# Performance work log

Hardware: AMD Instinct MI355X
Metric: run time of the kernel (lower is better)

Reference implementation:

```python
import jax, jax.numpy as jnp
import numpy as np

NUM_EMB = 512
EMB_DIM = 64
BETA = 0.25


def _conv(x, w, b, stride, pad):
    # x: NCHW, w: OIHW
    y = jax.lax.conv_general_dilated(
        x, w, window_strides=(stride, stride),
        padding=[(pad, pad), (pad, pad)],
        dimension_numbers=('NCHW', 'OIHW', 'NCHW'))
    return y + b[None, :, None, None]


def _deconv(x, w, b, stride, pad, k):
    # torch ConvTranspose2d weight is [in, out, kh, kw]; flip spatially,
    # swap to OIHW, and run a fractionally-strided (lhs-dilated) conv.
    wt = jnp.flip(w, axis=(2, 3)).transpose(1, 0, 2, 3)
    p = k - 1 - pad
    y = jax.lax.conv_general_dilated(
        x, wt, window_strides=(1, 1),
        padding=[(p, p), (p, p)],
        lhs_dilation=(stride, stride),
        dimension_numbers=('NCHW', 'OIHW', 'NCHW'))
    return y + b[None, :, None, None]


def setup_inputs() -> dict:
    key = jax.random.key(0)
    ks = jax.random.split(key, 16)
    s = 0.05
    inp = {
        'x': jax.random.normal(ks[0], (32, 3, 256, 256), jnp.float32),
        # encoder
        'w1': jax.random.normal(ks[1], (64, 3, 4, 4), jnp.float32) * s,
        'b1': jnp.zeros((64,), jnp.float32),
        'w2': jax.random.normal(ks[2], (128, 64, 4, 4), jnp.float32) * s,
        'b2': jnp.zeros((128,), jnp.float32),
        'w3': jax.random.normal(ks[3], (EMB_DIM, 128, 3, 3), jnp.float32) * s,
        'b3': jnp.zeros((EMB_DIM,), jnp.float32),
        # codebook, uniform(-1/N, 1/N) as in torch init
        'emb': jax.random.uniform(ks[4], (NUM_EMB, EMB_DIM), jnp.float32,
                                  -1.0 / NUM_EMB, 1.0 / NUM_EMB),
        # decoder (ConvTranspose2d weights: [in, out, kh, kw])
        'dw1': jax.random.normal(ks[5], (EMB_DIM, 128, 4, 4), jnp.float32) * s,
        'db1': jnp.zeros((128,), jnp.float32),
        'dw2': jax.random.normal(ks[6], (128, 64, 4, 4), jnp.float32) * s,
        'db2': jnp.zeros((64,), jnp.float32),
        'dw3': jax.random.normal(ks[7], (64, 3, 3, 3), jnp.float32) * s,
        'db3': jnp.zeros((3,), jnp.float32),
    }
    return inp


def _forward(x, w1, b1, w2, b2, w3, b3, emb, dw1, db1, dw2, db2, dw3, db3):
    # encoder
    h = jax.nn.relu(_conv(x, w1, b1, 2, 1))
    h = jax.nn.relu(_conv(h, w2, b2, 2, 1))
    z = jax.nn.relu(_conv(h, w3, b3, 1, 1))      # [B, D, H/4, W/4]
    z = z.transpose(0, 2, 3, 1)                   # NHWC
    # vector quantize
    flat = z.reshape(-1, EMB_DIM)                 # [N, D]
    d = (jnp.sum(flat * flat, axis=1, keepdims=True)
         - 2.0 * flat @ emb.T
         + jnp.sum(emb * emb, axis=1))            # [N, K]
    idx = jnp.argmin(d, axis=1)
    q = emb[idx].reshape(z.shape)
    sg = jax.lax.stop_gradient
    loss = jnp.mean((sg(q) - z) ** 2) + BETA * jnp.mean((q - sg(z)) ** 2)
    q = z + sg(q - z)                             # straight-through
    q = q.transpose(0, 3, 1, 2)                   # NCHW
    # decoder
    h = jax.nn.relu(_deconv(q, dw1, db1, 2, 1, 4))
    h = jax.nn.relu(_deconv(h, dw2, db2, 2, 1, 4))
    x_recon = jax.nn.sigmoid(_deconv(h, dw3, db3, 1, 1, 3))
    return x_recon, loss


def reference(x, w1, b1, w2, b2, w3, b3, emb, dw1, db1, dw2, db2, dw3, db3):
    return _forward(x, w1, b1, w2, b2, w3, b3, emb,
                    dw1, db1, dw2, db2, dw3, db3)
```

## Files before the change

### kernel.cpp

```cpp
#include <hip/hip_runtime.h>
#include <math.h>


typedef __attribute__((ext_vector_type(8))) short bf16x8;
typedef __attribute__((ext_vector_type(4))) float fx4;
typedef unsigned short ushort_t;
#define MFMA16(a, b, c) __builtin_amdgcn_mfma_f32_16x16x32_bf16(a, b, c, 0, 0, 0)

__device__ inline ushort_t f2bf(float f) {
    unsigned u = __float_as_uint(f);
    u += 0x7FFFu + ((u >> 16) & 1u);
    return (ushort_t)(u >> 16);
}
__device__ inline float bf2f(ushort_t h) {
    return __uint_as_float(((unsigned)h) << 16);
}

__device__ __forceinline__ void stage16(const ushort_t* g, ushort_t* l) {
#if __has_builtin(__builtin_amdgcn_global_load_lds)
    __builtin_amdgcn_global_load_lds(
        (const __attribute__((address_space(1))) unsigned int*)g,
        (__attribute__((address_space(3))) unsigned int*)l, 16, 0, 0);
#else
    int lane = threadIdx.x & 63;
    *(int4*)(l + lane * 8) = *(const int4*)g;
#endif
}

__device__ __forceinline__ int swz(int s) { return s ^ ((s >> 3) & 7); }
__device__ __forceinline__ bf16x8 sld(const ushort_t* sm, int gslot) {
    return *(const bf16x8*)(sm + (size_t)swz(gslot) * 8);
}

__device__ __forceinline__ void halo_do(
    ushort_t* __restrict__ buf, int B, int H, int W, int C8, int idx)
{
    int perim = 2 * W + 2 * (H - 2);
    int c8 = idx % C8;
    int t = idx / C8;
    int p = t % perim;
    int b = t / perim;
    int r, col;
    if (p < W) { r = 0; col = p; }
    else if (p < 2 * W) { r = H - 1; col = p - W; }
    else { int pp = p - 2 * W; r = 1 + (pp >> 1); col = (pp & 1) ? (W - 1) : 0; }
    size_t off = ((((size_t)b * H + r) * W + col) * C8 + c8) * 8;
    *(int4*)(buf + off) = (int4){0, 0, 0, 0};
}

__global__ __launch_bounds__(256) void halo3_k(
    ushort_t* __restrict__ xp, ushort_t* __restrict__ h2p, ushort_t* __restrict__ qpad)
{
    int i = blockIdx.x * 256 + threadIdx.x;
    if (i < 132096) halo_do(xp, 32, 130, 130, 8, i);
    else if (i < 265216) halo_do(h2p, 32, 66, 66, 16, i - 132096);
    else if (i < 331776) halo_do(qpad, 32, 66, 66, 8, i - 265216);
}
__global__ __launch_bounds__(256) void halo2_k(
    ushort_t* __restrict__ d1c, ushort_t* __restrict__ d2c)
{
    int i = blockIdx.x * 256 + threadIdx.x;
    if (i < 132096) halo_do(d1c, 16, 130, 130, 16, i);
    else if (i < 263680) halo_do(d2c, 16, 258, 258, 8, i - 132096);
}

__global__ __launch_bounds__(256) void cast_x4(
    const float* __restrict__ x, ushort_t* __restrict__ x4)
{
    if (blockIdx.x < 8192) {
        int i = blockIdx.x * 256 + threadIdx.x;
        int w = i & 255, h = (i >> 8) & 255, b = i >> 16;
        size_t base = ((size_t)b * 3 * 256 + h) * 256 + w;
        float v0 = x[base];
        float v1 = x[base + 65536];
        float v2 = x[base + 131072];
        uint2 o;
        o.x = (unsigned)f2bf(v0) | ((unsigned)f2bf(v1) << 16);
        o.y = (unsigned)f2bf(v2);
        *(uint2*)(x4 + ((size_t)(b * 258 + h + 1) * 258 + (w + 1)) * 4) = o;
    } else {
        int idx = (blockIdx.x - 8192) * 256 + threadIdx.x;
        if (idx >= 32 * 1032) return;
        int b = idx / 1032;
        int s = idx % 1032;
        int side = s / 258, c = s % 258;
        int r, col;
        if (side == 0) { r = 0; col = c; }
        else if (side == 1) { r = 257; col = c; }
        else if (side == 2) { r = c; col = 0; }
        else { r = c; col = 257; }
        *(uint2*)(x4 + ((size_t)(b * 258 + r) * 258 + col) * 4) = (uint2){0, 0};
    }
}

__global__ __launch_bounds__(256) void repack_all(
    const float* __restrict__ w1, const float* __restrict__ w2,
    const float* __restrict__ w3, const float* __restrict__ dw1,
    const float* __restrict__ dw2, const float* __restrict__ dw3,
    const float* __restrict__ emb,
    ushort_t* __restrict__ o1, ushort_t* __restrict__ o2,
    ushort_t* __restrict__ o3, ushort_t* __restrict__ od1,
    ushort_t* __restrict__ od2, ushort_t* __restrict__ od3,
    ushort_t* __restrict__ embb, float* __restrict__ se2,
    float* __restrict__ lac)
{
    int gi = blockIdx.x * 256 + threadIdx.x;
    if (gi < 4096) {
        int i = gi;
        int j = i & 7, lane = (i >> 3) & 63, tc = i >> 9;
        int c = tc & 1, t = tc >> 1;
        int co = t * 16 + (lane & 15);
        int k = c * 32 + (lane >> 4) * 8 + j;
        int kh = k >> 4, kw = (k >> 2) & 3, ci = k & 3;
        o1[i] = (ci < 3) ? f2bf(w1[((co * 3 + ci) * 4 + kh) * 4 + kw]) : (ushort_t)0;
    } else if (gi < 135168) {
        int i = gi - 4096;
        int j = i & 7, lane = (i >> 3) & 63, tc = i >> 9;
        int c = tc & 31, t = tc >> 5;
        int co = t * 16 + (lane & 15);
        int k = c * 32 + (lane >> 4) * 8 + j;
        int tap = k >> 6, ci = k & 63, kh = tap >> 2, kw = tap & 3;
        o2[i] = f2bf(w2[((co * 64 + ci) * 4 + kh) * 4 + kw]);
    } else if (gi < 208896) {
        int i = gi - 135168;
        int j = i & 7, lane = (i >> 3) & 63, tc = i >> 9;
        int c = tc % 36, t = tc / 36;
        int co = t * 16 + (lane & 15);
        int k = c * 32 + (lane >> 4) * 8 + j;
        int tap = k >> 7, ci = k & 127, kh = tap / 3, kw = tap % 3;
        o3[i] = f2bf(w3[((co * 128 + ci) * 3 + kh) * 3 + kw]);
    } else if (gi < 339968) {
        int i = gi - 208896;
        int j = i & 7, lane = (i >> 3) & 63, tc = i >> 9;
        int c = tc & 31, t = tc >> 5;
        int co = t * 16 + (lane & 15);
        int k = c * 32 + (lane >> 4) * 8 + j;
        int tap = k >> 6, ci = k & 63, kh = tap >> 2, kw = tap & 3;
        od1[i] = f2bf(dw1[((ci * 128 + co) * 4 + kh) * 4 + kw]);
    } else if (gi < 471040) {
        int i = gi - 339968;
        int j = i & 7, lane = (i >> 3) & 63, tc = i >> 9;
        int c = tc & 63, t = tc >> 6;
        int co = t * 16 + (lane & 15);
        int k = c * 32 + (lane >> 4) * 8 + j;
        int tap = k >> 7, ci = k & 127, kh = tap >> 2, kw = tap & 3;
        od2[i] = f2bf(dw2[((ci * 64 + co) * 4 + kh) * 4 + kw]);
    } else if (gi < 480256) {
        int i = gi - 471040;
        int j = i & 7, lane = (i >> 3) & 63, c = i >> 9;
        int co = lane & 15;
        int k = c * 32 + (lane >> 4) * 8 + j;
        int tap = k >> 6, ci = k & 63, kh = tap / 3, kw = tap % 3;
        od3[i] = (co < 3) ? f2bf(dw3[((ci * 3 + co) * 3 + kh) * 3 + kw]) : (ushort_t)0;
    } else if (gi < 513024) {
        int i = gi - 480256;
        int j = i & 7, lane = (i >> 3) & 63, c = (i >> 9) & 1, nt = i >> 10;
        int n = nt * 16 + (lane & 15);
        int k = c * 32 + (lane >> 4) * 8 + j;
        embb[i] = f2bf(emb[n * 64 + k]);
    } else if (gi < 513536) {
        int n = gi - 513024;
        const float* e = emb + n * 64;
        float s = 0.f;
        for (int d = 0; d < 64; ++d) s = fmaf(e[d], e[d], s);
        se2[n] = s;
    } else if (gi == 513536) {
        lac[0] = 0.f;
    }
}

__global__ __launch_bounds__(256) void conv1_mfma(
    const ushort_t* __restrict__ x4, const ushort_t* __restrict__ wr,
    const float* __restrict__ bias, ushort_t* __restrict__ xp)
{
    __shared__ ushort_t sm[4608];
    int tid = threadIdx.x;
    int wv = tid >> 6, lane = tid & 63;
    int n16 = lane & 15, quad = lane >> 4;
    int blk = blockIdx.x;
    int oh = blk & 127, b = blk >> 7;
    const ushort_t* gsrc = x4 + (size_t)(b * 258 + 2 * oh) * 1032;
    int sl = lane ^ ((lane >> 3) & 7);
    bf16x8 bfr[4][2];
    #pragma unroll
    for (int nt = 0; nt < 4; ++nt)
        #pragma unroll
        for (int c = 0; c < 2; ++c)
            bfr[nt][c] = *(const bf16x8*)(wr + ((size_t)(nt * 2 + c) * 64 + lane) * 8);
    for (int u = wv; u < 9; u += 4)
        stage16(gsrc + u * 512 + sl * 8, sm + u * 512);
    __syncthreads();

    fx4 acc[2][4];
    #pragma unroll
    for (int i = 0; i < 2; ++i)
        #pragma unroll
        for (int j = 0; j < 4; ++j) acc[i][j] = (fx4){0.f, 0.f, 0.f, 0.f};
    #pragma unroll
    for (int c = 0; c < 2; ++c) {
        int kh = 2 * c + (quad >> 1);
        int kwh = quad & 1;
        bf16x8 af[2];
        #pragma unroll
        for (int mt = 0; mt < 2; ++mt) {
            int ow = (wv * 2 + mt) * 16 + n16;
            af[mt] = sld(sm, kh * 129 + ow + kwh);
        }
        #pragma unroll
        for (int mt = 0; mt < 2; ++mt)
            #pragma unroll
            for (int nt = 0; nt < 4; ++nt)
                acc[mt][nt] = MFMA16(af[mt], bfr[nt][c], acc[mt][nt]);
    }
    #pragma unroll
    for (int nt = 0; nt < 4; ++nt) {
        int co = nt * 16 + n16;
        float bs = bias[co];
        #pragma unroll
        for (int mt = 0; mt < 2; ++mt) {
            #pragma unroll
            for (int r = 0; r < 4; ++r) {
                int ow = (wv * 2 + mt) * 16 + quad * 4 + r;
                xp[((size_t)(b * 130 + oh + 1) * 130 + (ow + 1)) * 64 + co] =
                    f2bf(fmaxf(acc[mt][nt][r] + bs, 0.f));
            }
        }
    }
}

__global__ __launch_bounds__(256, 2) void conv2_mfma(
    const ushort_t* __restrict__ xp, const ushort_t* __restrict__ wr,
    const float* __restrict__ bias, ushort_t* __restrict__ h2p)
{
    __shared__ ushort_t sm[33280];
    int tid = threadIdx.x;
    int wv = tid >> 6, lane = tid & 63;
    int n16 = lane & 15, quad = lane >> 4;
    int blk = blockIdx.x;
    int oh = blk & 63, b = blk >> 6;
    const ushort_t* gsrc = xp + (size_t)(b * 130 + 2 * oh) * 130 * 64;
    int sl = lane ^ ((lane >> 3) & 7);
    const ushort_t* w0 = wr + ((size_t)(wv * 2 + 0) * 32 * 64 + lane) * 8;
    const ushort_t* w1 = wr + ((size_t)(wv * 2 + 1) * 32 * 64 + lane) * 8;

    bf16x8 Bq[2][16];
    #pragma unroll
    for (int s = 0; s < 8; ++s) {
        Bq[0][2 * s]     = *(const bf16x8*)(w0 + (size_t)s * 512);
        Bq[0][2 * s + 1] = *(const bf16x8*)(w1 + (size_t)s * 512);
    }
    for (int u = wv; u < 65; u += 4)
        stage16(gsrc + (size_t)u * 512 + sl * 8, sm + u * 512);
    __syncthreads();

    fx4 acc[4][2];
    #pragma unroll
    for (int i = 0; i < 4; ++i)
        #pragma unroll
        for (int j = 0; j < 2; ++j) acc[i][j] = (fx4){0.f, 0.f, 0.f, 0.f};
    #pragma unroll
    for (int qb = 0; qb < 4; ++qb) {
        int cur = qb & 1;
        if (qb < 3) {
            #pragma unroll
            for (int s = 0; s < 8; ++s) {
                int st = (qb + 1) * 8 + s;
                Bq[cur ^ 1][2 * s]     = *(const bf16x8*)(w0 + (size_t)st * 512);
                Bq[cur ^ 1][2 * s + 1] = *(const bf16x8*)(w1 + (size_t)st * 512);
            }
        }
        #pragma unroll
        for (int s = 0; s < 8; ++s) {
            int step = qb * 8 + s, tap = step >> 1, ks = step & 1;
            int kh = tap >> 2, kw = tap & 3;
            bf16x8 af[4];
            #pragma unroll
            for (int mt = 0; mt < 4; ++mt) {
                int px = kw + 2 * (mt * 16 + n16);
                af[mt] = sld(sm, (kh * 130 + px) * 8 + ks * 4 + quad);
            }
            #pragma unroll
            for (int mt = 0; mt < 4; ++mt) {
                acc[mt][0] = MFMA16(af[mt], Bq[cur][2 * s], acc[mt][0]);
                acc[mt][1] = MFMA16(af[mt], Bq[cur][2 * s + 1], acc[mt][1]);
            }
        }
    }
    #pragma unroll
    for (int nt = 0; nt < 2; ++nt) {
        int co = (wv * 2 + nt) * 16 + n16;
        float bs = bias[co];
        #pragma unroll
        for (int mt = 0; mt < 4; ++mt) {
            #pragma unroll
            for (int r = 0; r < 4; ++r) {
                int ow = mt * 16 + quad * 4 + r;
                h2p[((size_t)(b * 66 + oh + 1) * 66 + (ow + 1)) * 128 + co] =
                    f2bf(fmaxf(acc[mt][nt][r] + bs, 0.f));
            }
        }
    }
}

__global__ __launch_bounds__(256, 2) void conv3_mfma(
    const ushort_t* __restrict__ hp, const ushort_t* __restrict__ wr,
    const float* __restrict__ bias, ushort_t* __restrict__ z)
{
    __shared__ ushort_t sm[25600];
    int tid = threadIdx.x;
    int wv = tid >> 6, lane = tid & 63;
    int n16 = lane & 15, quad = lane >> 4;
    int blk = blockIdx.x;
    int oh = blk & 63, b = blk >> 6;
    const ushort_t* gsrc = hp + (size_t)(b * 66 + oh) * 66 * 128;
    int sl = lane ^ ((lane >> 3) & 7);
    const ushort_t* wb = wr + ((size_t)wv * 36 * 64 + lane) * 8;
    bf16x8 Bb[36];
    #pragma unroll
    for (int s = 0; s < 36; ++s)
        Bb[s] = *(const bf16x8*)(wb + (size_t)s * 512);
    for (int u = wv; u < 50; u += 4)
        stage16(gsrc + (size_t)u * 512 + sl * 8, sm + u * 512);
    __syncthreads();

    fx4 acc[4];
    #pragma unroll
    for (int i = 0; i < 4; ++i) acc[i] = (fx4){0.f, 0.f, 0.f, 0.f};
    #pragma unroll
    for (int tap = 0; tap < 9; ++tap) {
        int kh = tap / 3, kw = tap % 3;
        #pragma unroll
        for (int ks = 0; ks < 4; ++ks) {
            bf16x8 af[4];
            #pragma unroll
            for (int mt = 0; mt < 4; ++mt) {
                int px = kw + mt * 16 + n16;
                af[mt] = sld(sm, (kh * 66 + px) * 16 + ks * 4 + quad);
            }
            #pragma unroll
            for (int mt = 0; mt < 4; ++mt)
                acc[mt] = MFMA16(af[mt], Bb[tap * 4 + ks], acc[mt]);
        }
    }
    int co = wv * 16 + n16;
    float bs = bias[co];
    #pragma unroll
    for (int mt = 0; mt < 4; ++mt) {
        #pragma unroll
        for (int r = 0; r < 4; ++r) {
            int ow = mt * 16 + quad * 4 + r;
            z[((size_t)(b * 64 + oh) * 64 + ow) * 64 + co] =
                f2bf(fmaxf(acc[mt][r] + bs, 0.f));
        }
    }
}

__global__ __launch_bounds__(256) void vq_mfma(
    const ushort_t* __restrict__ z, const ushort_t* __restrict__ embb,
    const float* __restrict__ emb, const float* __restrict__ se2g,
    ushort_t* __restrict__ qpad, float* __restrict__ loss_acc)
{
    __shared__ ushort_t smz[16384];
    __shared__ float sse2[512];
    __shared__ float red[256];
    int tid = threadIdx.x;
    int wv = tid >> 6, lane = tid & 63;
    int n16 = lane & 15, quad = lane >> 4;
    int blk = blockIdx.x;
    const ushort_t* gsrc = z + (size_t)blk * 16384;
    int sl = lane ^ ((lane >> 3) & 7);
    for (int u = wv; u < 32; u += 4)
        stage16(gsrc + (size_t)u * 512 + sl * 8, smz + u * 512);
    for (int i = tid; i < 512; i += 256) sse2[i] = se2g[i];
    __syncthreads();

    bf16x8 a[4][2];
    #pragma unroll
    for (int mt = 0; mt < 4; ++mt)
        #pragma unroll
        for (int ks = 0; ks < 2; ++ks)
            a[mt][ks] = sld(smz, (wv * 64 + mt * 16 + n16) * 8 + ks * 4 + quad);

    float best[4][4];
    int bid[4][4];
    #pragma unroll
    for (int mt = 0; mt < 4; ++mt)
        #pragma unroll
        for (int r = 0; r < 4; ++r) { best[mt][r] = 1e30f; bid[mt][r] = 0; }

    for (int nt = 0; nt < 32; ++nt) {
        bf16x8 b0 = *(const bf16x8*)(embb + ((size_t)(nt * 2 + 0) * 64 + lane) * 8);
        bf16x8 b1 = *(const bf16x8*)(embb + ((size_t)(nt * 2 + 1) * 64 + lane) * 8);
        float s2 = sse2[nt * 16 + n16];
        int myn = nt * 16 + n16;
        #pragma unroll
        for (int mt = 0; mt < 4; ++mt) {
            fx4 acc = (fx4){0.f, 0.f, 0.f, 0.f};
            acc = MFMA16(a[mt][0], b0, acc);
            acc = MFMA16(a[mt][1], b1, acc);
            #pragma unroll
            for (int r = 0; r < 4; ++r) {
                float sc = fmaf(-2.f, acc[r], s2);
                if (sc < best[mt][r]) { best[mt][r] = sc; bid[mt][r] = myn; }
            }
        }
    }

    float lsum = 0.f;
    #pragma unroll
    for (int mt = 0; mt < 4; ++mt) {
        #pragma unroll
        for (int r = 0; r < 4; ++r) {
            float bs = best[mt][r];
            int bi = bid[mt][r];
            #pragma unroll
            for (int st = 1; st < 16; st <<= 1) {
                float os = __shfl_xor(bs, st, 64);
                int oi = __shfl_xor(bi, st, 64);
                if (os < bs || (os == bs && oi < bi)) { bs = os; bi = oi; }
            }
            int ml = wv * 64 + mt * 16 + quad * 4 + r;
            int pos = blk * 256 + ml;
            int b = pos >> 12, h = (pos >> 6) & 63, w = pos & 63;
            float4 ev = *(const float4*)(emb + (size_t)bi * 64 + n16 * 4);
            int slot = ml * 8 + (n16 >> 1);
            const ushort_t* zp = smz + (size_t)swz(slot) * 8 + (n16 & 1) * 4;
            float d0 = ev.x - bf2f(zp[0]);
            float d1 = ev.y - bf2f(zp[1]);
            float d2 = ev.z - bf2f(zp[2]);
            float d3 = ev.w - bf2f(zp[3]);
            lsum = fmaf(d0, d0, lsum);
            lsum = fmaf(d1, d1, lsum);
            lsum = fmaf(d2, d2, lsum);
            lsum = fmaf(d3, d3, lsum);
            uint2 o;
            o.x = (unsigned)f2bf(ev.x) | ((unsigned)f2bf(ev.y) << 16);
            o.y = (unsigned)f2bf(ev.z) | ((unsigned)f2bf(ev.w) << 16);
            *(uint2*)(qpad + ((size_t)(b * 66 + h + 1) * 66 + (w + 1)) * 64 + n16 * 4) = o;
        }
    }
    red[tid] = lsum;
    __syncthreads();
    for (int s = 128; s > 0; s >>= 1) {
        if (tid < s) red[tid] += red[tid + s];
        __syncthreads();
    }
    if (tid == 0) atomicAdd(loss_acc, red[0]);
}

__global__ void loss_fin_k(const float* __restrict__ acc, float* __restrict__ out)
{
    out[0] = 1.25f * acc[0] / 8388608.0f;
}

__global__ __launch_bounds__(256, 2) void deconv1_mfma(
    const ushort_t* __restrict__ q, const ushort_t* __restrict__ wr,
    const float* __restrict__ bias, ushort_t* __restrict__ d1)
{
    __shared__ ushort_t sm[8704];
    int tid = threadIdx.x;
    int wv = tid >> 6, lane = tid & 63;
    int n16 = lane & 15, quad = lane >> 4;
    int blk = blockIdx.x;
    int oh = blk & 127, b = blk >> 7;
    int h0 = (oh + 1) & 1;
    int ihp0 = ((oh + 1 - h0) >> 1) + 1;
    const ushort_t* gsrc = q + (size_t)(b * 66 + ihp0 - 1) * 66 * 64;
    int sl = lane ^ ((lane >> 3) & 7);
    int pw = wv & 1, ng = wv >> 1;
    int q0 = 1 - pw;
    bf16x8 Bb[4][8];
    #pragma unroll
    for (int nt = 0; nt < 4; ++nt) {
        const ushort_t* wb = wr + ((size_t)(ng * 4 + nt) * 32 * 64 + lane) * 8;
        #pragma unroll
        for (int t2 = 0; t2 < 2; ++t2)
            #pragma unroll
            for (int t3 = 0; t3 < 2; ++t3)
                #pragma unroll
                for (int ks = 0; ks < 2; ++ks) {
                    int tap = (h0 + 2 * t2) * 4 + (q0 + 2 * t3);
                    Bb[nt][t2 * 4 + t3 * 2 + ks] =
                        *(const bf16x8*)(wb + (size_t)(tap * 2 + ks) * 512);
                }
    }
    for (int u = wv; u < 17; u += 4)
        stage16(gsrc + (size_t)u * 512 + sl * 8, sm + u * 512);
    __syncthreads();

    fx4 acc[4][4];
    #pragma unroll
    for (int i = 0; i < 4; ++i)
        #pragma unroll
        for (int j = 0; j < 4; ++j) acc[i][j] = (fx4){0.f, 0.f, 0.f, 0.f};
    #pragma unroll
    for (int t2 = 0; t2 < 2; ++t2) {
        int lrow = 1 - t2;
        #pragma unroll
        for (int t3 = 0; t3 < 2; ++t3) {
            int cadd = pw + (t3 == 0 ? 1 : 0);
            #pragma unroll
            for (int ks = 0; ks < 2; ++ks) {
                bf16x8 af[4];
                #pragma unroll
                for (int mt = 0; mt < 4; ++mt) {
                    int px = cadd + mt * 16 + n16;
                    af[mt] = sld(sm, (lrow * 66 + px) * 8 + ks * 4 + quad);
                }
                #pragma unroll
                for (int mt = 0; mt < 4; ++mt)
                    #pragma unroll
                    for (int nt = 0; nt < 4; ++nt)
                        acc[mt][nt] = MFMA16(af[mt], Bb[nt][t2 * 4 + t3 * 2 + ks], acc[mt][nt]);
            }
        }
    }
    #pragma unroll
    for (int nt = 0; nt < 4; ++nt) {
        int co = (ng * 4 + nt) * 16 + n16;
        float bs = bias[co];
        #pragma unroll
        for (int mt = 0; mt < 4; ++mt) {
            #pragma unroll
            for (int r = 0; r < 4; ++r) {
                int ow = 2 * (mt * 16 + quad * 4 + r) + pw;
                d1[((size_t)(b * 130 + oh + 1) * 130 + (ow + 1)) * 128 + co] =
                    f2bf(fmaxf(acc[mt][nt][r] + bs, 0.f));
            }
        }
    }
}

__global__ __launch_bounds__(256, 2) void deconv2_mfma(
    const ushort_t* __restrict__ d1, const ushort_t* __restrict__ wr,
    const float* __restrict__ bias, ushort_t* __restrict__ d2)
{
    __shared__ ushort_t sm[33280];
    int tid = threadIdx.x;
    int wv = tid >> 6, lane = tid & 63;
    int n16 = lane & 15, quad = lane >> 4;
    int blk = blockIdx.x;
    int oh = blk & 255, b = blk >> 8;
    int h0 = (oh + 1) & 1;
    int ihp0 = ((oh + 1 - h0) >> 1) + 1;
    const ushort_t* gsrc = d1 + (size_t)(b * 130 + ihp0 - 1) * 130 * 128;
    int sl = lane ^ ((lane >> 3) & 7);
    int pw = wv & 1, ng = wv >> 1;
    int q0 = 1 - pw;
    bf16x8 Bb[2][16];
    #pragma unroll
    for (int nt = 0; nt < 2; ++nt) {
        const ushort_t* wb = wr + ((size_t)(ng * 2 + nt) * 64 * 64 + lane) * 8;
        #pragma unroll
        for (int t2 = 0; t2 < 2; ++t2)
            #pragma unroll
            for (int t3 = 0; t3 < 2; ++t3) {
                int tap = (h0 + 2 * t2) * 4 + (q0 + 2 * t3);
                #pragma unroll
                for (int ks = 0; ks < 4; ++ks)
                    Bb[nt][t2 * 8 + t3 * 4 + ks] =
                        *(const bf16x8*)(wb + (size_t)(tap * 4 + ks) * 512);
            }
    }
    for (int u = wv; u < 65; u += 4)
        stage16(gsrc + (size_t)u * 512 + sl * 8, sm + u * 512);
    __syncthreads();

    fx4 acc[8][2];
    #pragma unroll
    for (int i = 0; i < 8; ++i)
        #pragma unroll
        for (int j = 0; j < 2; ++j) acc[i][j] = (fx4){0.f, 0.f, 0.f, 0.f};
    #pragma unroll
    for (int t2 = 0; t2 < 2; ++t2) {
        int lrow = 1 - t2;
        #pragma unroll
        for (int t3 = 0; t3 < 2; ++t3) {
            int cadd = pw + (t3 == 0 ? 1 : 0);
            #pragma unroll
            for (int ks = 0; ks < 4; ++ks) {
                #pragma unroll
                for (int mt = 0; mt < 8; ++mt) {
                    int px = cadd + mt * 16 + n16;
                    bf16x8 af = sld(sm, (lrow * 130 + px) * 16 + ks * 4 + quad);
                    acc[mt][0] = MFMA16(af, Bb[0][t2 * 8 + t3 * 4 + ks], acc[mt][0]);
                    acc[mt][1] = MFMA16(af, Bb[1][t2 * 8 + t3 * 4 + ks], acc[mt][1]);
                }
            }
        }
    }
    #pragma unroll
    for (int nt = 0; nt < 2; ++nt) {
        int co = (ng * 2 + nt) * 16 + n16;
        float bs = bias[co];
        #pragma unroll
        for (int mt = 0; mt < 8; ++mt) {
            #pragma unroll
            for (int r = 0; r < 4; ++r) {
                int ow = 2 * (mt * 16 + quad * 4 + r) + pw;
                d2[((size_t)(b * 258 + oh + 1) * 258 + (ow + 1)) * 64 + co] =
                    f2bf(fmaxf(acc[mt][nt][r] + bs, 0.f));
            }
        }
    }
}

__global__ __launch_bounds__(256) void deconv3_mfma(
    const ushort_t* __restrict__ d2, const ushort_t* __restrict__ wr,
    const float* __restrict__ bias, float* __restrict__ out)
{
    __shared__ ushort_t sm[26112];
    int tid = threadIdx.x;
    int wv = tid >> 6, lane = tid & 63;
    int n16 = lane & 15, quad = lane >> 4;
    int blk = blockIdx.x;
    int half = blk & 1;
    int oh = (blk >> 1) & 255;
    int b = blk >> 9;
    int sl = lane ^ ((lane >> 3) & 7);
    bf16x8 Bb[18];
    #pragma unroll
    for (int s = 0; s < 18; ++s)
        Bb[s] = *(const bf16x8*)(wr + ((size_t)s * 64 + lane) * 8);
    for (int u = wv; u < 51; u += 4) {
        int c = u / 17, uu = u - c * 17;
        const ushort_t* gsrc = d2 + ((size_t)(b * 258 + oh + c) * 258 + half * 128) * 64;
        stage16(gsrc + (size_t)uu * 512 + sl * 8, sm + c * 8704 + uu * 512);
    }
    __syncthreads();

    fx4 acc[2];
    #pragma unroll
    for (int i = 0; i < 2; ++i) acc[i] = (fx4){0.f, 0.f, 0.f, 0.f};
    #pragma unroll
    for (int tap = 0; tap < 9; ++tap) {
        int kh = tap / 3, kw = tap % 3;
        int c = 2 - kh;
        #pragma unroll
        for (int ks = 0; ks < 2; ++ks) {
            bf16x8 af[2];
            #pragma unroll
            for (int mt = 0; mt < 2; ++mt) {
                int px = (2 - kw) + (wv * 2 + mt) * 16 + n16;
                af[mt] = sld(sm, c * 1088 + px * 8 + ks * 4 + quad);
            }
            #pragma unroll
            for (int mt = 0; mt < 2; ++mt)
                acc[mt] = MFMA16(af[mt], Bb[tap * 2 + ks], acc[mt]);
        }
    }
    int co = n16;
    if (co < 3) {
        float bs = bias[co];
        #pragma unroll
        for (int mt = 0; mt < 2; ++mt) {
            int ow0 = half * 128 + (wv * 2 + mt) * 16 + quad * 4;
            float4 v;
            v.x = 1.f / (1.f + __expf(-(acc[mt][0] + bs)));
            v.y = 1.f / (1.f + __expf(-(acc[mt][1] + bs)));
            v.z = 1.f / (1.f + __expf(-(acc[mt][2] + bs)));
            v.w = 1.f / (1.f + __expf(-(acc[mt][3] + bs)));
            *(float4*)(out + (((size_t)b * 3 + co) * 256 + oh) * 256 + ow0) = v;
        }
    }
}

extern "C" void kernel_launch(void* const* d_in, const int* in_sizes, int n_in,
                              void* d_out, int out_size, void* d_ws, size_t ws_size,
                              hipStream_t stream)
{
    const float* x   = (const float*)d_in[0];
    const float* w1  = (const float*)d_in[1];
    const float* b1  = (const float*)d_in[2];
    const float* w2  = (const float*)d_in[3];
    const float* b2  = (const float*)d_in[4];
    const float* w3  = (const float*)d_in[5];
    const float* b3  = (const float*)d_in[6];
    const float* emb = (const float*)d_in[7];
    const float* dw1 = (const float*)d_in[8];
    const float* db1 = (const float*)d_in[9];
    const float* dw2 = (const float*)d_in[10];
    const float* db2 = (const float*)d_in[11];
    const float* dw3 = (const float*)d_in[12];
    const float* db3 = (const float*)d_in[13];
    float* xout = (float*)d_out;

    ushort_t* shared = (ushort_t*)d_ws;
    ushort_t* xp   = shared;
    ushort_t* h2p  = shared + 34611200;
    ushort_t* d1c  = shared;
    ushort_t* d2c  = shared + 34611200;
    ushort_t* x4   = shared + 94252544;
    ushort_t* zb   = shared + 102772736;
    ushort_t* qpad = zb + 8388608;
    ushort_t* wr1  = qpad + 8921088;
    ushort_t* wr2  = wr1  + 4096;
    ushort_t* wr3  = wr2  + 131072;
    ushort_t* wd1  = wr3  + 73728;
    ushort_t* wd2  = wd1  + 131072;
    ushort_t* wd3  = wd2  + 131072;
    ushort_t* embb = wd3  + 9216;
    float*    se2  = (float*)(embb + 32768);
    float*    lac  = se2 + 512;

    repack_all<<<2007, 256, 0, stream>>>(w1, w2, w3, dw1, dw2, dw3, emb,
                                         wr1, wr2, wr3, wd1, wd2, wd3,
                                         embb, se2, lac);
    cast_x4 <<<8321, 256, 0, stream>>>(x, x4);
    halo3_k <<<1296, 256, 0, stream>>>(xp, h2p, qpad);

    conv1_mfma<<<4096, 256, 0, stream>>>(x4, wr1, b1, xp);
    conv2_mfma<<<2048, 256, 0, stream>>>(xp, wr2, b2, h2p);
    conv3_mfma<<<2048, 256, 0, stream>>>(h2p, wr3, b3, zb);
    vq_mfma   <<<512,  256, 0, stream>>>(zb, embb, emb, se2, qpad, lac);
    loss_fin_k<<<1, 1, 0, stream>>>(lac, xout + 6291456);

    halo2_k<<<1030, 256, 0, stream>>>(d1c, d2c);

    for (int c0 = 0; c0 < 32; c0 += 16) {
        deconv1_mfma<<<2048, 256, 0, stream>>>(qpad + (size_t)c0 * 278784, wd1, db1, d1c);
        deconv2_mfma<<<4096, 256, 0, stream>>>(d1c, wd2, db2, d2c);
        deconv3_mfma<<<8192, 256, 0, stream>>>(d2c, wd3, db3, xout + (size_t)c0 * 196608);
    }
}
```

Before: 592.2 us.

## Switch deconv2 to 32x32x16 MFMA with double-buffered per-tap weight loads

Rewrites deconv2 to use 32x32x16 bf16 MFMA tiles. Each wave now covers half the output columns and all 64 output channels, instead of all columns and 32 channels. The dw2 weight prepack layout is changed to match. Weights are loaded per tap into a double-buffered register set, overlapped with compute, rather than all held at once. The accumulator is initialized with the bias. This aims to raise MFMA efficiency and cut register pressure at the cost of more global weight loads per block.

```diff
diff --git a/kernel.cpp b/kernel.cpp
--- a/kernel.cpp
+++ b/kernel.cpp
@@ -4,8 +4,10 @@
 
 typedef __attribute__((ext_vector_type(8))) short bf16x8;
 typedef __attribute__((ext_vector_type(4))) float fx4;
+typedef __attribute__((ext_vector_type(16))) float fx16;
 typedef unsigned short ushort_t;
 #define MFMA16(a, b, c) __builtin_amdgcn_mfma_f32_16x16x32_bf16(a, b, c, 0, 0, 0)
+#define MFMA32(a, b, c) __builtin_amdgcn_mfma_f32_32x32x16_bf16(a, b, c, 0, 0, 0)
 
 __device__ inline ushort_t f2bf(float f) {
     unsigned u = __float_as_uint(f);
@@ -139,11 +141,11 @@
         od1[i] = f2bf(dw1[((ci * 128 + co) * 4 + kh) * 4 + kw]);
     } else if (gi < 471040) {
         int i = gi - 339968;
-        int j = i & 7, lane = (i >> 3) & 63, tc = i >> 9;
-        int c = tc & 63, t = tc >> 6;
-        int co = t * 16 + (lane & 15);
-        int k = c * 32 + (lane >> 4) * 8 + j;
-        int tap = k >> 7, ci = k & 127, kh = tap >> 2, kw = tap & 3;
+        int j = i & 7, lane = (i >> 3) & 63, f = i >> 9;
+        int kk = f & 7, tap = (f >> 3) & 15, nt = f >> 7;
+        int co = nt * 32 + (lane & 31);
+        int ci = kk * 16 + (lane >> 5) * 8 + j;
+        int kh = tap >> 2, kw = tap & 3;
         od2[i] = f2bf(dw2[((ci * 64 + co) * 4 + kh) * 4 + kw]);
     } else if (gi < 480256) {
         int i = gi - 471040;
@@ -538,68 +540,82 @@
     __shared__ ushort_t sm[33280];
     int tid = threadIdx.x;
     int wv = tid >> 6, lane = tid & 63;
-    int n16 = lane & 15, quad = lane >> 4;
+    int r31 = lane & 31, hi = lane >> 5;
     int blk = blockIdx.x;
     int oh = blk & 255, b = blk >> 8;
     int h0 = (oh + 1) & 1;
     int ihp0 = ((oh + 1 - h0) >> 1) + 1;
     const ushort_t* gsrc = d1 + (size_t)(b * 130 + ihp0 - 1) * 130 * 128;
     int sl = lane ^ ((lane >> 3) & 7);
-    int pw = wv & 1, ng = wv >> 1;
+    int pw = wv & 1, mh = wv >> 1;
     int q0 = 1 - pw;
+
+    int taps[4];
+    #pragma unroll
+    for (int g = 0; g < 4; ++g)
+        taps[g] = (h0 + 2 * (g >> 1)) * 4 + (q0 + 2 * (g & 1));
+
     bf16x8 Bb[2][16];
     #pragma unroll
-    for (int nt = 0; nt < 2; ++nt) {
-        const ushort_t* wb = wr + ((size_t)(ng * 2 + nt) * 64 * 64 + lane) * 8;
-        #pragma unroll
-        for (int t2 = 0; t2 < 2; ++t2)
-            #pragma unroll
-            for (int t3 = 0; t3 < 2; ++t3) {
-                int tap = (h0 + 2 * t2) * 4 + (q0 + 2 * t3);
-                #pragma unroll
-                for (int ks = 0; ks < 4; ++ks)
-                    Bb[nt][t2 * 8 + t3 * 4 + ks] =
-                        *(const bf16x8*)(wb + (size_t)(tap * 4 + ks) * 512);
-            }
-    }
+    for (int nt = 0; nt < 2; ++nt)
+        #pragma unroll
+        for (int kk = 0; kk < 8; ++kk)
+            Bb[0][nt * 8 + kk] = *(const bf16x8*)(
+                wr + (size_t)((nt * 16 + taps[0]) * 8 + kk) * 512 + lane * 8);
+
     for (int u = wv; u < 65; u += 4)
         stage16(gsrc + (size_t)u * 512 + sl * 8, sm + u * 512);
     __syncthreads();
 
-    fx4 acc[8][2];
-    #pragma unroll
-    for (int i = 0; i < 8; ++i)
-        #pragma unroll
-        for (int j = 0; j < 2; ++j) acc[i][j] = (fx4){0.f, 0.f, 0.f, 0.f};
-    #pragma unroll
-    for (int t2 = 0; t2 < 2; ++t2) {
+    fx16 acc[2][2];
+    #pragma unroll
+    for (int nt = 0; nt < 2; ++nt) {
+        float bv = bias[nt * 32 + r31];
+        #pragma unroll
+        for (int mt = 0; mt < 2; ++mt)
+            #pragma unroll
+            for (int r = 0; r < 16; ++r) acc[mt][nt][r] = bv;
+    }
+
+    #pragma unroll
+    for (int g = 0; g < 4; ++g) {
+        int cur = g & 1;
+        if (g < 3) {
+            int tapn = taps[g + 1];
+            #pragma unroll
+            for (int nt = 0; nt < 2; ++nt)
+                #pragma unroll
+                for (int kk = 0; kk < 8; ++kk)
+                    Bb[cur ^ 1][nt * 8 + kk] = *(const bf16x8*)(
+                        wr + (size_t)((nt * 16 + tapn) * 8 + kk) * 512 + lane * 8);
+        }
+        int t2 = g >> 1, t3 = g & 1;
         int lrow = 1 - t2;
-        #pragma unroll
-        for (int t3 = 0; t3 < 2; ++t3) {
-            int cadd = pw + (t3 == 0 ? 1 : 0);
-            #pragma unroll
-            for (int ks = 0; ks < 4; ++ks) {
-                #pragma unroll
-                for (int mt = 0; mt < 8; ++mt) {
-                    int px = cadd + mt * 16 + n16;
-                    bf16x8 af = sld(sm, (lrow * 130 + px) * 16 + ks * 4 + quad);
-                    acc[mt][0] = MFMA16(af, Bb[0][t2 * 8 + t3 * 4 + ks], acc[mt][0]);
-                    acc[mt][1] = MFMA16(af, Bb[1][t2 * 8 + t3 * 4 + ks], acc[mt][1]);
-                }
-            }
-        }
-    }
+        int cadd = pw + (t3 == 0 ? 1 : 0);
+        int base = (lrow * 130 + cadd + mh * 64 + r31) * 16 + hi;
+        #pragma unroll
+        for (int kk = 0; kk < 8; ++kk) {
+            bf16x8 a0 = sld(sm, base + kk * 2);
+            bf16x8 a1 = sld(sm, base + 512 + kk * 2);
+            acc[0][0] = MFMA32(a0, Bb[cur][kk],     acc[0][0]);
+            acc[0][1] = MFMA32(a0, Bb[cur][8 + kk], acc[0][1]);
+            acc[1][0] = MFMA32(a1, Bb[cur][kk],     acc[1][0]);
+            acc[1][1] = MFMA32(a1, Bb[cur][8 + kk], acc[1][1]);
+        }
+    }
+
     #pragma unroll
     for (int nt = 0; nt < 2; ++nt) {
-        int co = (ng * 2 + nt) * 16 + n16;
-        float bs = bias[co];
-        #pragma unroll
-        for (int mt = 0; mt < 8; ++mt) {
-            #pragma unroll
-            for (int r = 0; r < 4; ++r) {
-                int ow = 2 * (mt * 16 + quad * 4 + r) + pw;
+        int co = nt * 32 + r31;
+        #pragma unroll
+        for (int mt = 0; mt < 2; ++mt) {
+            #pragma unroll
+            for (int r = 0; r < 16; ++r) {
+                int row = (r & 3) + 8 * (r >> 2) + 4 * hi;
+                int t = mh * 64 + mt * 32 + row;
+                int ow = 2 * t + pw;
                 d2[((size_t)(b * 258 + oh + 1) * 258 + (ow + 1)) * 64 + co] =
-                    f2bf(fmaxf(acc[mt][nt][r] + bs, 0.f));
+                    f2bf(fmaxf(acc[mt][nt][r], 0.f));
             }
         }
     }
```

New measurement: 681.0 us. 15.0% more time.

## Split deconv2 rows into halves and stream weights to raise occupancy

Applied to the files above, without the earlier changes.

Each deconv2 block now handles half an output row (64 input columns), which halves the LDS staging buffer and doubles the grid. Waves are remapped so each covers all four output-channel tiles over two M tiles, and weights are loaded from global per tap in small chunks instead of being held in 32 registers up front. The aim is to cut register and LDS pressure so four blocks fit per CU, at the cost of repeated weight loads from global/L2 and some halo re-staging.

```diff
diff --git a/kernel.cpp b/kernel.cpp
--- a/kernel.cpp
+++ b/kernel.cpp
@@ -531,73 +531,81 @@
     }
 }
 
-__global__ __launch_bounds__(256, 2) void deconv2_mfma(
+__global__ __launch_bounds__(256, 4) void deconv2_mfma(
     const ushort_t* __restrict__ d1, const ushort_t* __restrict__ wr,
     const float* __restrict__ bias, ushort_t* __restrict__ d2)
 {
-    __shared__ ushort_t sm[33280];
+    __shared__ ushort_t sm[17408];
     int tid = threadIdx.x;
     int wv = tid >> 6, lane = tid & 63;
     int n16 = lane & 15, quad = lane >> 4;
     int blk = blockIdx.x;
-    int oh = blk & 255, b = blk >> 8;
+    int half = blk & 1;
+    int oh = (blk >> 1) & 255;
+    int b = blk >> 9;
     int h0 = (oh + 1) & 1;
     int ihp0 = ((oh + 1 - h0) >> 1) + 1;
-    const ushort_t* gsrc = d1 + (size_t)(b * 130 + ihp0 - 1) * 130 * 128;
     int sl = lane ^ ((lane >> 3) & 7);
-    int pw = wv & 1, ng = wv >> 1;
+    int pw = wv & 1, mg = wv >> 1;
     int q0 = 1 - pw;
-    bf16x8 Bb[2][16];
-    #pragma unroll
-    for (int nt = 0; nt < 2; ++nt) {
-        const ushort_t* wb = wr + ((size_t)(ng * 2 + nt) * 64 * 64 + lane) * 8;
-        #pragma unroll
-        for (int t2 = 0; t2 < 2; ++t2)
-            #pragma unroll
-            for (int t3 = 0; t3 < 2; ++t3) {
-                int tap = (h0 + 2 * t2) * 4 + (q0 + 2 * t3);
-                #pragma unroll
-                for (int ks = 0; ks < 4; ++ks)
-                    Bb[nt][t2 * 8 + t3 * 4 + ks] =
-                        *(const bf16x8*)(wb + (size_t)(tap * 4 + ks) * 512);
-            }
-    }
-    for (int u = wv; u < 65; u += 4)
-        stage16(gsrc + (size_t)u * 512 + sl * 8, sm + u * 512);
+    for (int u = wv; u < 34; u += 4) {
+        int r = u / 17, uu = u - r * 17;
+        const ushort_t* gsrc = d1 +
+            ((size_t)(b * 130 + ihp0 - 1 + r) * 130 + half * 64) * 128;
+        stage16(gsrc + (size_t)uu * 512 + sl * 8, sm + u * 512);
+    }
     __syncthreads();
 
-    fx4 acc[8][2];
-    #pragma unroll
-    for (int i = 0; i < 8; ++i)
-        #pragma unroll
-        for (int j = 0; j < 2; ++j) acc[i][j] = (fx4){0.f, 0.f, 0.f, 0.f};
+    fx4 acc[2][4];
+    #pragma unroll
+    for (int i = 0; i < 2; ++i)
+        #pragma unroll
+        for (int j = 0; j < 4; ++j) acc[i][j] = (fx4){0.f, 0.f, 0.f, 0.f};
+
     #pragma unroll
     for (int t2 = 0; t2 < 2; ++t2) {
         int lrow = 1 - t2;
         #pragma unroll
         for (int t3 = 0; t3 < 2; ++t3) {
             int cadd = pw + (t3 == 0 ? 1 : 0);
-            #pragma unroll
-            for (int ks = 0; ks < 4; ++ks) {
+            int tap = (h0 + 2 * t2) * 4 + (q0 + 2 * t3);
+            #pragma unroll
+            for (int kh2 = 0; kh2 < 2; ++kh2) {
+                bf16x8 Bb[8];
                 #pragma unroll
-                for (int mt = 0; mt < 8; ++mt) {
-                    int px = cadd + mt * 16 + n16;
-                    bf16x8 af = sld(sm, (lrow * 130 + px) * 16 + ks * 4 + quad);
-                    acc[mt][0] = MFMA16(af, Bb[0][t2 * 8 + t3 * 4 + ks], acc[mt][0]);
-                    acc[mt][1] = MFMA16(af, Bb[1][t2 * 8 + t3 * 4 + ks], acc[mt][1]);
+                for (int nt = 0; nt < 4; ++nt)
+                    #pragma unroll
+                    for (int k2 = 0; k2 < 2; ++k2)
+                        Bb[nt * 2 + k2] = *(const bf16x8*)(
+                            wr + ((size_t)(nt * 64 + tap * 4 + kh2 * 2 + k2) * 64 + lane) * 8);
+                #pragma unroll
+                for (int k2 = 0; k2 < 2; ++k2) {
+                    int ks = kh2 * 2 + k2;
+                    bf16x8 af[2];
+                    #pragma unroll
+                    for (int mt = 0; mt < 2; ++mt) {
+                        int px = cadd + (mg * 2 + mt) * 16 + n16;
+                        af[mt] = sld(sm, lrow * 1088 + px * 16 + ks * 4 + quad);
+                    }
+                    #pragma unroll
+                    for (int mt = 0; mt < 2; ++mt)
+                        #pragma unroll
+                        for (int nt = 0; nt < 4; ++nt)
+                            acc[mt][nt] = MFMA16(af[mt], Bb[nt * 2 + k2], acc[mt][nt]);
                 }
             }
         }
     }
     #pragma unroll
-    for (int nt = 0; nt < 2; ++nt) {
-        int co = (ng * 2 + nt) * 16 + n16;
+    for (int nt = 0; nt < 4; ++nt) {
+        int co = nt * 16 + n16;
         float bs = bias[co];
         #pragma unroll
-        for (int mt = 0; mt < 8; ++mt) {
+        for (int mt = 0; mt < 2; ++mt) {
             #pragma unroll
             for (int r = 0; r < 4; ++r) {
-                int ow = 2 * (mt * 16 + quad * 4 + r) + pw;
+                int t = half * 64 + (mg * 2 + mt) * 16 + quad * 4 + r;
+                int ow = 2 * t + pw;
                 d2[((size_t)(b * 258 + oh + 1) * 258 + (ow + 1)) * 64 + co] =
                     f2bf(fmaxf(acc[mt][nt][r] + bs, 0.f));
             }
@@ -719,7 +727,7 @@
 
     for (int c0 = 0; c0 < 32; c0 += 16) {
         deconv1_mfma<<<2048, 256, 0, stream>>>(qpad + (size_t)c0 * 278784, wd1, db1, d1c);
-        deconv2_mfma<<<4096, 256, 0, stream>>>(d1c, wd2, db2, d2c);
+        deconv2_mfma<<<8192, 256, 0, stream>>>(d1c, wd2, db2, d2c);
         deconv3_mfma<<<8192, 256, 0, stream>>>(d2c, wd3, db3, xout + (size_t)c0 * 196608);
     }
 }
```

New measurement: 681.5 us. 1.15x slower.
